# Performance work log

Hardware: AMD Instinct MI355X
Metric: run time of the kernel (lower is better)

Reference implementation:

```python
import jax, jax.numpy as jnp
import numpy as np
from jax import lax

STRIDE = (1, 1)
PADDING = ((1, 1), (1, 1))
DILATION = (1, 1)
GROUPS = 1


def setup_inputs() -> dict:
    key = jax.random.key(0)
    k1, k2, k3, k4, k5 = jax.random.split(key, 5)
    # quantized int8-ish activations/weights stored as float (as in the torch module)
    x = jax.random.randint(k1, (32, 128, 56, 56), -128, 128).astype(jnp.float32)
    weight_int = jax.random.randint(k2, (256, 128, 3, 3), -128, 128).astype(jnp.float32)
    bias_int = jax.random.randint(k3, (256,), -1024, 1024).astype(jnp.float32)
    A = jax.random.randint(k4, (256,), 1, 32768)  # per-channel requant multiplier
    N = jax.random.randint(k5, (256,), 16, 25)    # per-channel shift
    return {
        "x": x,
        "weight_int": weight_int,
        "bias_int": bias_int,
        "A": A,
        "N": N,
        "out_min": 0,
        "out_max": 255,
    }


def reference(x, weight_int, bias_int, A, N, out_min, out_max):
    # emulate torch's x.int().float() truncation casts
    xq = jnp.trunc(x)
    wq = jnp.trunc(weight_int)
    bq = jnp.trunc(bias_int)
    out = lax.conv_general_dilated(
        xq, wq,
        window_strides=STRIDE,
        padding=PADDING,
        rhs_dilation=DILATION,
        feature_group_count=GROUPS,
        dimension_numbers=("NCHW", "OIHW", "NCHW"),
    )
    out = jnp.round(out + bq[None, :, None, None])
    # out *= A ; out >>= N  (torch float rshift == divide by 2**N)
    Af = A.astype(jnp.float32)[None, :, None, None]
    Nf = N.astype(jnp.float32)[None, :, None, None]
    out = out * Af / jnp.exp2(Nf)
    if out_min >= 0:
        out = jnp.clip(jnp.round(out), float(out_min), float(out_max))
    return out
```

## Files before the change

### kernel.cpp

```cpp
#include <hip/hip_runtime.h>
#include <stdint.h>

typedef int   v4i __attribute__((ext_vector_type(4)));
typedef float v4f __attribute__((ext_vector_type(4)));

#define XT_H_STRIDE (66*128)
#define XT_N_STRIDE (58*66*128)
#define XT_BYTES    (32*58*66*128)
#define WQ_BYTES    (256*1152)

__device__ __forceinline__ void gload16(const void* g, void* l) {
  __builtin_amdgcn_global_load_lds(
      (const __attribute__((address_space(1))) void*)g,
      (__attribute__((address_space(3))) void*)l, 16, 0, 0);
}

__global__ __launch_bounds__(256) void xform_x(const float* __restrict__ x,
                                               char* __restrict__ xt) {
  __shared__ int LB[56 * 33];
  int bid = blockIdx.x;
  int n  = bid / 58;
  int hp = bid - n * 58;
  int t  = threadIdx.x;
  int srch = hp - 1;
  bool rowok = (srch >= 0) && (srch < 56);
  char* dstrow = xt + (size_t)n * XT_N_STRIDE + (size_t)hp * XT_H_STRIDE;

  if (rowok) {
    const float* rb = x + ((size_t)(n * 128) * 56 + srch) * 56;
#pragma unroll
    for (int u0 = 0; u0 < 2; ++u0) {
      int u  = t + u0 * 256;
      int wb = u & 15;
      int cb = u >> 4;
      int w0 = wb * 4, ci0 = cb * 4;
      if (w0 < 56) {
        int dw[4] = {0, 0, 0, 0};
#pragma unroll
        for (int i = 0; i < 4; ++i) {
          v4f f = *(const v4f*)(rb + (size_t)(ci0 + i) * 3136 + w0);
#pragma unroll
          for (int j = 0; j < 4; ++j)
            dw[j] |= (((int)f[j]) & 255) << (8 * i);
        }
#pragma unroll
        for (int j = 0; j < 4; ++j)
          LB[(w0 + j) * 33 + cb] = dw[j];
      }
    }
    __syncthreads();
    for (int c = t; c < 528; c += 256) {
      int wp  = c >> 3;
      int cio = c & 7;
      int srw = wp - 1;
      v4i v = {0, 0, 0, 0};
      if (srw >= 0 && srw < 56) {
#pragma unroll
        for (int k = 0; k < 4; ++k) v[k] = LB[srw * 33 + cio * 4 + k];
      }
      *(v4i*)(dstrow + c * 16) = v;
    }
  } else {
    v4i z = {0, 0, 0, 0};
    for (int c = t; c < 528; c += 256) *(v4i*)(dstrow + c * 16) = z;
  }
}

__global__ __launch_bounds__(256) void xform_w(const float* __restrict__ wsrc,
                                               const int* __restrict__ Aq,
                                               const int* __restrict__ Nq,
                                               char* __restrict__ wq3,
                                               float* __restrict__ scale) {
  int idx = blockIdx.x * 256 + threadIdx.x;
  int co = idx / 1152;
  int k  = idx - co * 1152;
  int g  = k >> 7;
  int ci = k & 127;
  int kh = g / 3;
  int kw = g - 3 * kh;
  float f = wsrc[(size_t)(co * 128 + ci) * 9 + kh * 3 + kw];
  int kt    = k >> 6;
  int mhalf = co >> 7;
  int chunk = (k >> 4) & 3;
  int row   = co & 127;
  int col   = k & 15;
  wq3[(((kt * 2 + mhalf) * 4 + chunk) * 128 + row) * 16 + col] = (signed char)(int)f;
  if (idx < 256) {
    scale[idx] = (float)Aq[idx] * exp2f(-(float)Nq[idx]);
  }
}

__global__ __launch_bounds__(256, 2) void qconv_gemm(
    const char* __restrict__ xt, const char* __restrict__ wq3,
    const float* __restrict__ bias, const float* __restrict__ scale,
    const int* __restrict__ pmin, const int* __restrict__ pmax,
    float* __restrict__ out) {
  __shared__ __align__(16) char Bp[4 * 8448];
  __shared__ __align__(16) char As[3][8192];

  int bid = blockIdx.x;
  int xcd = bid & 7;
  int q   = bid >> 3;
  int mt  = q & 1;
  int nt  = xcd * 112 + (q >> 1);
  int n   = nt / 28;
  int ht  = nt - n * 28;
  int h0  = ht * 2;
  int m0  = mt * 128;

  int t  = threadIdx.x;
  int wv = t >> 6;
  int ln = t & 63;
  int quad = ln >> 4;
  int l16  = ln & 15;
  int wm = wv & 1, wn = wv >> 1;

  const char* xb    = xt + (size_t)n * XT_N_STRIDE + (size_t)h0 * XT_H_STRIDE;
  const char* wbase = wq3 + mt * 8192;

  for (int it = 0; it < 9; ++it) {
    int s = t + it * 256;
    if (s < 2112) {
      int row = s / 528;
      int rr  = s - row * 528;
      int w   = rr >> 3;
      int cq  = rr & 7;
      gload16(xb + row * XT_H_STRIDE + w * 128 + ((cq ^ (w & 7)) << 4),
              Bp + it * 4096 + wv * 1024);
    }
  }
#pragma unroll
  for (int kk = 0; kk < 2; ++kk) {
    const char* src = wbase + kk * 16384;
    gload16(src + t * 16,        As[kk] + wv * 1024);
    gload16(src + 4096 + t * 16, As[kk] + 4096 + wv * 1024);
  }
  asm volatile("s_waitcnt vmcnt(2)" ::: "memory");
  asm volatile("s_barrier" ::: "memory");

  v4i a[4], b[4], bn[4];
  {
    const char* bb = Bp + wn * XT_H_STRIDE + l16 * 128 + ((quad ^ (l16 & 7)) << 4);
#pragma unroll
    for (int j = 0; j < 4; ++j)
      b[j] = *(const v4i*)(bb + j * 2048);
  }

  v4i acc[4][4];
#pragma unroll
  for (int i = 0; i < 4; ++i)
#pragma unroll
    for (int j = 0; j < 4; ++j) {
      v4i z = {0, 0, 0, 0};
      acc[i][j] = z;
    }

#pragma unroll
  for (int kt = 0; kt < 18; ++kt) {
    const int p = kt % 3;

    if (kt < 16) {
      const char* src = wbase + (kt + 2) * 16384;
      char* dst = As[(kt + 2) % 3];
      gload16(src + t * 16,        dst + wv * 1024);
      gload16(src + 4096 + t * 16, dst + 4096 + wv * 1024);
    }

    const char* ab = As[p] + quad * 2048 + (wm * 64 + l16) * 16;
#pragma unroll
    for (int i = 0; i < 4; ++i)
      a[i] = *(const v4i*)(ab + i * 256);

    __builtin_amdgcn_sched_barrier(0);
    asm volatile("s_waitcnt lgkmcnt(0)" ::: "memory");
    __builtin_amdgcn_sched_barrier(0);

    __builtin_amdgcn_s_setprio(1);
#pragma unroll
    for (int i = 0; i < 4; ++i)
#pragma unroll
      for (int j = 0; j < 4; ++j)
        acc[i][j] = __builtin_amdgcn_mfma_i32_16x16x64_i8(a[i], b[j], acc[i][j], 0, 0, 0);
    __builtin_amdgcn_s_setprio(0);

    if (kt < 17) {
      const int kn  = kt + 1;
      const int pn  = kn & 1;
      const int gn  = kn >> 1;
      const int khn = gn / 3;
      const int kwn = gn - 3 * khn;
      int bswzn = (((pn << 2) + quad) ^ ((l16 + kwn) & 7)) << 4;
      const char* bbn = Bp + (wn + khn) * XT_H_STRIDE + (l16 + kwn) * 128 + bswzn;
#pragma unroll
      for (int j = 0; j < 4; ++j)
        bn[j] = *(const v4i*)(bbn + j * 2048);

      __builtin_amdgcn_sched_barrier(0);
      if (kt < 16) {
        asm volatile("s_waitcnt vmcnt(2)" ::: "memory");
      } else {
        asm volatile("s_waitcnt vmcnt(0)" ::: "memory");
      }
      asm volatile("s_barrier" ::: "memory");

#pragma unroll
      for (int u = 0; u < 4; ++u) b[u] = bn[u];
    }
  }

  float mn = (float)pmin[0];
  float mx = (float)pmax[0];
#pragma unroll
  for (int i = 0; i < 4; ++i) {
    int co_b = m0 + wm * 64 + i * 16 + quad * 4;
#pragma unroll
    for (int r = 0; r < 4; ++r) {
      int co = co_b + r;
      float bs = bias[co];
      float sc = scale[co];
#pragma unroll
      for (int j = 0; j < 4; ++j) {
        int sl = wn * 64 + j * 16 + l16;
        int w  = sl & 63;
        int dh = sl >> 6;
        if (w < 56) {
          float f = (float)acc[i][j][r] + bs;
          f = rintf(f * sc);
          f = fminf(fmaxf(f, mn), mx);
          out[(((size_t)n * 256 + co) * 56 + (h0 + dh)) * 56 + w] = f;
        }
      }
    }
  }
}

extern "C" void kernel_launch(void* const* d_in, const int* in_sizes, int n_in,
                              void* d_out, int out_size, void* d_ws, size_t ws_size,
                              hipStream_t stream) {
  const float* x  = (const float*)d_in[0];
  const float* w  = (const float*)d_in[1];
  const float* b  = (const float*)d_in[2];
  const int*   Aq = (const int*)d_in[3];
  const int*   Nq = (const int*)d_in[4];
  const int*   mn = (const int*)d_in[5];
  const int*   mx = (const int*)d_in[6];
  float* out = (float*)d_out;

  char*  xt    = (char*)d_ws;
  char*  wq3   = xt + XT_BYTES;
  float* scale = (float*)(wq3 + WQ_BYTES);

  hipLaunchKernelGGL(xform_x, dim3(32 * 58), dim3(256), 0, stream, x, xt);
  hipLaunchKernelGGL(xform_w, dim3(1152), dim3(256), 0, stream, w, Aq, Nq, wq3, scale);
  hipLaunchKernelGGL(qconv_gemm, dim3(1792), dim3(256), 0, stream,
                     xt, wq3, b, scale, mn, mx, out);
}
```

Before: 196.1 us.

## Stream per-step input tiles into double-buffered LDS instead of resident halo

The GEMM kernel no longer loads the full 4-row halo input slab into LDS once with a triple-buffered weight ring. Instead it reloads a small 8 KB input tile per K step, double-buffered alongside the weight tile. This cuts LDS use enough to raise the occupancy hint from 2 to 4 blocks per CU. The cost is re-fetching overlapping input rows from global/L2 on every step, two barriers per iteration, and the loss of the priority and scheduling hints.

Measured after the change: 189.4 us. -3.4%, faster.

```diff
diff --git a/kernel.cpp b/kernel.cpp
--- a/kernel.cpp
+++ b/kernel.cpp
@@ -90,13 +90,13 @@
   }
 }
 
-__global__ __launch_bounds__(256, 2) void qconv_gemm(
+__global__ __launch_bounds__(256, 4) void qconv_gemm(
     const char* __restrict__ xt, const char* __restrict__ wq3,
     const float* __restrict__ bias, const float* __restrict__ scale,
     const int* __restrict__ pmin, const int* __restrict__ pmax,
     float* __restrict__ out) {
-  __shared__ __align__(16) char Bp[4 * 8448];
-  __shared__ __align__(16) char As[3][8192];
+  __shared__ __align__(16) char As[2][8192];
+  __shared__ __align__(16) char Bs[2][8192];
 
   int bid = blockIdx.x;
   int xcd = bid & 7;
@@ -115,36 +115,28 @@
   int l16  = ln & 15;
   int wm = wv & 1, wn = wv >> 1;
 
-  const char* xb    = xt + (size_t)n * XT_N_STRIDE + (size_t)h0 * XT_H_STRIDE;
-  const char* wbase = wq3 + mt * 8192;
-
-  for (int it = 0; it < 9; ++it) {
-    int s = t + it * 256;
-    if (s < 2112) {
-      int row = s / 528;
-      int rr  = s - row * 528;
-      int w   = rr >> 3;
-      int cq  = rr & 7;
-      gload16(xb + row * XT_H_STRIDE + w * 128 + ((cq ^ (w & 7)) << 4),
-              Bp + it * 4096 + wv * 1024);
-    }
-  }
-#pragma unroll
-  for (int kk = 0; kk < 2; ++kk) {
-    const char* src = wbase + kk * 16384;
-    gload16(src + t * 16,        As[kk] + wv * 1024);
-    gload16(src + 4096 + t * 16, As[kk] + 4096 + wv * 1024);
-  }
-  asm volatile("s_waitcnt vmcnt(2)" ::: "memory");
+  const char* xb = xt + (size_t)n * XT_N_STRIDE + (size_t)h0 * XT_H_STRIDE;
+
+  int boffv[2];
+#pragma unroll
+  for (int u = 0; u < 2; ++u) {
+    int s  = wv * 64 + u * 256 + ln;
+    int sp = s >> 2;
+    int ck = s & 3;
+    boffv[u] = (sp >> 6) * XT_H_STRIDE + (sp & 63) * 128 + ((ck ^ (sp & 3)) << 4);
+  }
+  const int aoff = quad * 2048 + (wm * 64 + l16) * 16;
+  const int boff = (wn * 64 + l16) * 64 + ((quad ^ (l16 & 3)) << 4);
+
+  {
+    const char* a0 = wq3 + (size_t)mt * 8192;
+    gload16(a0 + t * 16,        As[0] + wv * 1024);
+    gload16(a0 + 4096 + t * 16, As[0] + 4096 + wv * 1024);
+    gload16(xb + boffv[0],      Bs[0] + wv * 1024);
+    gload16(xb + boffv[1],      Bs[0] + 4096 + wv * 1024);
+  }
+  asm volatile("s_waitcnt vmcnt(0)" ::: "memory");
   asm volatile("s_barrier" ::: "memory");
-
-  v4i a[4], b[4], bn[4];
-  {
-    const char* bb = Bp + wn * XT_H_STRIDE + l16 * 128 + ((quad ^ (l16 & 7)) << 4);
-#pragma unroll
-    for (int j = 0; j < 4; ++j)
-      b[j] = *(const v4i*)(bb + j * 2048);
-  }
 
   v4i acc[4][4];
 #pragma unroll
@@ -157,55 +149,40 @@
 
 #pragma unroll
   for (int kt = 0; kt < 18; ++kt) {
-    const int p = kt % 3;
-
-    if (kt < 16) {
-      const char* src = wbase + (kt + 2) * 16384;
-      char* dst = As[(kt + 2) % 3];
-      gload16(src + t * 16,        dst + wv * 1024);
-      gload16(src + 4096 + t * 16, dst + 4096 + wv * 1024);
-    }
-
-    const char* ab = As[p] + quad * 2048 + (wm * 64 + l16) * 16;
+    const int buf = kt & 1;
+
+    asm volatile("s_barrier" ::: "memory");
+    if (kt < 17) {
+      const int kn  = kt + 1;
+      const int gn  = kn >> 1;
+      const int pn  = kn & 1;
+      const int khn = gn / 3;
+      const int kwn = gn - 3 * khn;
+      const int koff = khn * XT_H_STRIDE + kwn * 128 + pn * 64;
+      const char* an = wq3 + (size_t)(kn * 2 + mt) * 8192;
+      const char* bn = xb + koff;
+      gload16(an + t * 16,        As[buf ^ 1] + wv * 1024);
+      gload16(an + 4096 + t * 16, As[buf ^ 1] + 4096 + wv * 1024);
+      gload16(bn + boffv[0],      Bs[buf ^ 1] + wv * 1024);
+      gload16(bn + boffv[1],      Bs[buf ^ 1] + 4096 + wv * 1024);
+      asm volatile("s_waitcnt vmcnt(4)" ::: "memory");
+    } else {
+      asm volatile("s_waitcnt vmcnt(0)" ::: "memory");
+    }
+    asm volatile("s_barrier" ::: "memory");
+
+    v4i a[4], b[4];
 #pragma unroll
     for (int i = 0; i < 4; ++i)
-      a[i] = *(const v4i*)(ab + i * 256);
-
-    __builtin_amdgcn_sched_barrier(0);
-    asm volatile("s_waitcnt lgkmcnt(0)" ::: "memory");
-    __builtin_amdgcn_sched_barrier(0);
-
-    __builtin_amdgcn_s_setprio(1);
+      a[i] = *(const v4i*)(As[buf] + aoff + i * 256);
+#pragma unroll
+    for (int j = 0; j < 4; ++j)
+      b[j] = *(const v4i*)(Bs[buf] + boff + j * 1024);
 #pragma unroll
     for (int i = 0; i < 4; ++i)
 #pragma unroll
       for (int j = 0; j < 4; ++j)
         acc[i][j] = __builtin_amdgcn_mfma_i32_16x16x64_i8(a[i], b[j], acc[i][j], 0, 0, 0);
-    __builtin_amdgcn_s_setprio(0);
-
-    if (kt < 17) {
-      const int kn  = kt + 1;
-      const int pn  = kn & 1;
-      const int gn  = kn >> 1;
-      const int khn = gn / 3;
-      const int kwn = gn - 3 * khn;
-      int bswzn = (((pn << 2) + quad) ^ ((l16 + kwn) & 7)) << 4;
-      const char* bbn = Bp + (wn + khn) * XT_H_STRIDE + (l16 + kwn) * 128 + bswzn;
-#pragma unroll
-      for (int j = 0; j < 4; ++j)
-        bn[j] = *(const v4i*)(bbn + j * 2048);
-
-      __builtin_amdgcn_sched_barrier(0);
-      if (kt < 16) {
-        asm volatile("s_waitcnt vmcnt(2)" ::: "memory");
-      } else {
-        asm volatile("s_waitcnt vmcnt(0)" ::: "memory");
-      }
-      asm volatile("s_barrier" ::: "memory");
-
-#pragma unroll
-      for (int u = 0; u < 4; ++u) b[u] = bn[u];
-    }
   }
 
   float mn = (float)pmin[0];
```
